# Kernel optimization log

Measured on AMD Instinct MI355X. Metric: run time of the kernel, lower is better.

The kernel has to match this reference:

```python
import jax, jax.numpy as jnp
import numpy as np

H, A, V = 8, 32, 32
NODE_IN, EDGE_IN, NODE_OUT, EDGE_OUT = 128, 64, 128, 64


def setup_inputs() -> dict:
    key = jax.random.key(0)
    ks = jax.random.split(key, 8)
    B, N = 1, 384
    s = lambda fan: 1.0 / np.sqrt(fan).astype(np.float32)
    nodes = jax.random.normal(ks[0], (B, NODE_IN, N), jnp.float32)
    edges = jax.random.normal(ks[1], (B, EDGE_IN, N, N), jnp.float32)
    mask = jax.random.randint(ks[2], (B, N), 0, 2).astype(bool)
    W_q = jax.random.normal(ks[3], (A * H, NODE_IN), jnp.float32) * s(NODE_IN)
    W_k = jax.random.normal(ks[4], (A * H, NODE_IN + EDGE_IN), jnp.float32) * s(NODE_IN + EDGE_IN)
    W_v = jax.random.normal(ks[5], (V * H, NODE_IN + EDGE_IN), jnp.float32) * s(NODE_IN + EDGE_IN)
    W_o = jax.random.normal(ks[6], (NODE_OUT, V * H), jnp.float32) * s(V * H)
    W_e = jax.random.normal(ks[7], (EDGE_OUT, V * H + EDGE_IN), jnp.float32) * s(V * H + EDGE_IN)
    return dict(nodes=nodes, edges=edges, mask=mask, W_q=W_q, W_k=W_k, W_v=W_v, W_o=W_o, W_e=W_e)


def reference(nodes, edges, mask, W_q, W_k, W_v, W_o, W_e):
    B, C, N = nodes.shape
    # 1x1 convs are channel matmuls
    query = jnp.einsum('oc,bcn->bon', W_q, nodes)                      # [B, H*A, N]
    node_edges = jnp.concatenate(
        [jnp.broadcast_to(nodes[:, :, :, None], (B, C, N, N)), edges], axis=1)  # [B, C+E, N, N]
    key = jnp.einsum('oc,bcij->boij', W_k, node_edges)                 # [B, H*A, N, N]
    value = jnp.einsum('oc,bcij->boij', W_v, node_edges).reshape(B, H, V, N, N)
    # elementwise QK: query broadcast over column axis j
    sim = (query[:, :, :, None] * key).reshape(B, H, A, N, N).sum(axis=2)
    sim = sim / jnp.sqrt(jnp.asarray(A, sim.dtype))                    # [B, H, N, N]
    sim = jnp.where(mask[:, None, None, :], sim, -jnp.inf)
    sim = jax.nn.softmax(sim, axis=-1)
    mm = (mask[:, None, :, None] & mask[:, None, None, :]).astype(sim.dtype)  # [B,1,N,N]
    sim = sim * mm
    value = value * mm[:, None]
    node_features = jnp.einsum('bhij,bhvij->bhvi', sim, value).reshape(B, H * V, N)
    node_out = jnp.einsum('od,bdn->bon', W_o, node_features)           # [B, node_out, N]
    # symmetrized edge features: (f_i + f_j) / 2, then concat raw edges
    ef = (node_features[:, :, :, None] + node_features[:, :, None, :]) * 0.5  # [B,H*V,N,N]
    ef = jnp.concatenate([ef, edges], axis=1)
    edge_out = jnp.einsum('oc,bcij->boij', W_e, ef)                    # [B, edge_out, N, N]
    return node_out, edge_out
```

## Files before the change

kernel.cpp:

```cpp
#include <hip/hip_runtime.h>
#include <math.h>

#define NN 384
#define NSQ (NN*NN)

#define WS_MASKF 0
#define WS_C1    384
#define WS_P     3456
#define WS_VN    200064
#define WS_T     298368
#define WS_GH    494976
#define WS_WT    519552
#define WS_WOT   523648
#define WS_WVE   556416
#define WS_WEN   572800

typedef short short8 __attribute__((ext_vector_type(8)));
typedef float f32x4 __attribute__((ext_vector_type(4)));

__device__ __forceinline__ unsigned short f2bf(float x) {
    unsigned u = __float_as_uint(x);
    return (unsigned short)((u + 0x7FFFu + ((u >> 16) & 1u)) >> 16);
}

__global__ __launch_bounds__(256) void k_proj(
    const float* __restrict__ nodes, const float* __restrict__ Wq,
    const float* __restrict__ Wk, const float* __restrict__ Wv,
    const float* __restrict__ Wo, const float* __restrict__ We,
    const unsigned int* __restrict__ mi, float* __restrict__ ws) {
    int tid = threadIdx.x;
    if (blockIdx.x >= 48) {
        if (blockIdx.x == 48) {
            __shared__ int bytemode;
            if (tid == 0) bytemode = 0;
            __syncthreads();
            unsigned v0 = mi[tid];
            unsigned v1 = (tid < 128) ? mi[256 + tid] : 0u;
            if (v0 > 1u || v1 > 1u) bytemode = 1;
            __syncthreads();
            float* maskf = ws + WS_MASKF;
            for (int j = tid; j < NN; j += 256) {
                int on;
                if (bytemode) on = (((const unsigned char*)mi)[j] != 0);
                else          on = (mi[j] != 0u);
                maskf[j] = on ? 1.0f : 0.0f;
            }
        } else if (blockIdx.x == 49) {
            float* Wt = ws + WS_WT;
            for (int idx = tid; idx < 4096; idx += 256) {
                int c = idx >> 6, o = idx & 63;
                Wt[c * 64 + o] = We[o * 320 + 256 + c];
            }
        } else if (blockIdx.x == 50) {
            float* WoT = ws + WS_WOT;
            for (int idx = tid; idx < 32768; idx += 256) {
                int dd = idx >> 7, o = idx & 127;
                WoT[dd * 128 + o] = Wo[o * 256 + dd];
            }
        } else if (blockIdx.x == 51) {
            float* WvE = ws + WS_WVE;
            for (int idx = tid; idx < 16384; idx += 256) {
                int c = idx >> 8, d = idx & 255;
                WvE[c * 256 + d] = Wv[d * 192 + 128 + c];
            }
        } else {
            float* WeN = ws + WS_WEN;
            for (int idx = tid; idx < 16384; idx += 256) {
                int dd = idx >> 6, o = idx & 63;
                WeN[dd * 64 + o] = We[o * 320 + dd];
            }
        }
        return;
    }
    float* c1_ws = ws + WS_C1;
    float* P_ws  = ws + WS_P;
    float* vn_ws = ws + WS_VN;
    int i0 = blockIdx.x * 8;
    __shared__ float nl[128][8];
    __shared__ float q_l[256][8];
    __shared__ float qk_l[256][8];
    for (int idx = tid; idx < 1024; idx += 256) {
        int m = idx >> 3, ii = idx & 7;
        nl[m][ii] = nodes[m * NN + i0 + ii];
    }
    __syncthreads();
    int o = tid;
    float aq[8], ak[8], av[8];
#pragma unroll
    for (int ii = 0; ii < 8; ii++) { aq[ii] = 0.f; ak[ii] = 0.f; av[ii] = 0.f; }
#pragma unroll 4
    for (int m = 0; m < 128; m++) {
        float wq = Wq[o * 128 + m];
        float wk = Wk[o * 192 + m];
        float wv = Wv[o * 192 + m];
#pragma unroll
        for (int ii = 0; ii < 8; ii++) {
            float nv = nl[m][ii];
            aq[ii] = fmaf(wq, nv, aq[ii]);
            ak[ii] = fmaf(wk, nv, ak[ii]);
            av[ii] = fmaf(wv, nv, av[ii]);
        }
    }
#pragma unroll
    for (int ii = 0; ii < 8; ii++) {
        vn_ws[(size_t)(i0 + ii) * 256 + o] = av[ii];
        q_l[o][ii]  = aq[ii];
        qk_l[o][ii] = aq[ii] * ak[ii];
    }
    __syncthreads();
    if (tid < 64) {
        int h = tid >> 3, ii = tid & 7;
        float s = 0.f;
        for (int a = 0; a < 32; a++) s += qk_l[h * 32 + a][ii];
        c1_ws[(i0 + ii) * 8 + h] = s;
    }
    for (int rep = 0; rep < 2; rep++) {
        int idx = rep * 256 + tid;
        int c = idx & 63, h = idx >> 6;
        float ap[8];
#pragma unroll
        for (int ii = 0; ii < 8; ii++) ap[ii] = 0.f;
        for (int a = 0; a < 32; a++) {
            float w = Wk[(h * 32 + a) * 192 + 128 + c];
#pragma unroll
            for (int ii = 0; ii < 8; ii++)
                ap[ii] = fmaf(q_l[h * 32 + a][ii], w, ap[ii]);
        }
#pragma unroll
        for (int ii = 0; ii < 8; ii++)
            P_ws[(size_t)(i0 + ii) * 512 + c * 8 + h] = ap[ii];
    }
}

__global__ __launch_bounds__(512) void k_attn(
    const float* __restrict__ edges, const float* __restrict__ ws_ro,
    float* __restrict__ T_ws) {
    __shared__ __align__(16) unsigned short epad_h[64 * 392];
    __shared__ __align__(16) float sT2[NN * 8];
    const float* maskf = ws_ro + WS_MASKF;
    const float* c1w   = ws_ro + WS_C1;
    const float* Pw    = ws_ro + WS_P;
    int i = blockIdx.x;
    int tid = threadIdx.x;
    int wv = tid >> 6, ln = tid & 63;
    float mask_i = maskf[i];

    if (tid < NN) {
        int j = tid;
        const float* eb = edges + (size_t)i * NN + j;
        const float* Pi = Pw + (size_t)i * 512;
        float acc[8];
#pragma unroll
        for (int h = 0; h < 8; h++) acc[h] = 0.f;
#pragma unroll
        for (int cb = 0; cb < 4; cb++) {
            float ev[16];
#pragma unroll
            for (int t = 0; t < 16; t++)
                ev[t] = eb[(size_t)(cb * 16 + t) * NSQ];
#pragma unroll
            for (int t = 0; t < 16; t++) {
                int c = cb * 16 + t;
                epad_h[c * 392 + j] = f2bf(ev[t]);
                const float* Pc = Pi + c * 8;
#pragma unroll
                for (int h = 0; h < 8; h++) acc[h] = fmaf(Pc[h], ev[t], acc[h]);
            }
        }
        float mj = maskf[j];
        const float* c1i = c1w + i * 8;
        float sv[8];
#pragma unroll
        for (int h = 0; h < 8; h++) {
            float s = (c1i[h] + acc[h]) * 0.17677669529663687f;
            sv[h] = (mj != 0.0f) ? s : -1e30f;
        }
        *reinterpret_cast<float4*>(&sT2[j * 8])     = make_float4(sv[0], sv[1], sv[2], sv[3]);
        *reinterpret_cast<float4*>(&sT2[j * 8 + 4]) = make_float4(sv[4], sv[5], sv[6], sv[7]);
    }
    __syncthreads();
    float v[6];
    {
        int h = wv;
#pragma unroll
        for (int k = 0; k < 6; k++) v[k] = sT2[(ln + 64 * k) * 8 + h];
    }
    __syncthreads();
    {
        int h = wv;
        float m = v[0];
#pragma unroll
        for (int k = 1; k < 6; k++) m = fmaxf(m, v[k]);
#pragma unroll
        for (int s = 1; s < 64; s <<= 1) m = fmaxf(m, __shfl_xor(m, s));
        float ex[6]; float sum = 0.f;
#pragma unroll
        for (int k = 0; k < 6; k++) { ex[k] = __expf(v[k] - m); sum += ex[k]; }
#pragma unroll
        for (int s = 1; s < 64; s <<= 1) sum += __shfl_xor(sum, s);
        float fac = mask_i / sum;
        unsigned short* s_bf = reinterpret_cast<unsigned short*>(sT2);
#pragma unroll
        for (int k = 0; k < 6; k++)
            s_bf[h * 392 + ln + 64 * k] = f2bf(ex[k] * fac);
    }
    __syncthreads();
    if (tid < 64) {
        const unsigned short* s_bf = reinterpret_cast<const unsigned short*>(sT2);
        int L = tid;
        int nc   = L & 15;
        int quad = L >> 4;
        int hrow = nc & 7;
        f32x4 acc0 = {0.f, 0.f, 0.f, 0.f};
        f32x4 acc1 = {0.f, 0.f, 0.f, 0.f};
        f32x4 acc2 = {0.f, 0.f, 0.f, 0.f};
        f32x4 acc3 = {0.f, 0.f, 0.f, 0.f};
#pragma unroll
        for (int s = 0; s < 12; s++) {
            int jb = s * 32 + quad * 8;
            short8 a = *reinterpret_cast<const short8*>(&s_bf[hrow * 392 + jb]);
            short8 b0 = *reinterpret_cast<const short8*>(&epad_h[(0 * 16 + nc) * 392 + jb]);
            short8 b1 = *reinterpret_cast<const short8*>(&epad_h[(1 * 16 + nc) * 392 + jb]);
            short8 b2 = *reinterpret_cast<const short8*>(&epad_h[(2 * 16 + nc) * 392 + jb]);
            short8 b3 = *reinterpret_cast<const short8*>(&epad_h[(3 * 16 + nc) * 392 + jb]);
            acc0 = __builtin_amdgcn_mfma_f32_16x16x32_bf16(a, b0, acc0, 0, 0, 0);
            acc1 = __builtin_amdgcn_mfma_f32_16x16x32_bf16(a, b1, acc1, 0, 0, 0);
            acc2 = __builtin_amdgcn_mfma_f32_16x16x32_bf16(a, b2, acc2, 0, 0, 0);
            acc3 = __builtin_amdgcn_mfma_f32_16x16x32_bf16(a, b3, acc3, 0, 0, 0);
        }
        if (L < 32) {
            float* To = T_ws + (size_t)i * 512;
#pragma unroll
            for (int r = 0; r < 4; r++) {
                int h = quad * 4 + r;
                To[h * 64 +  0 + nc] = acc0[r];
                To[h * 64 + 16 + nc] = acc1[r];
                To[h * 64 + 32 + nc] = acc2[r];
                To[h * 64 + 48 + nc] = acc3[r];
            }
        }
    }
}

__global__ __launch_bounds__(256) void k_nf(
    const float* __restrict__ ws_ro, float* __restrict__ gh_ws,
    float* __restrict__ out) {
    const float* maskf = ws_ro + WS_MASKF;
    const float* vn_ws = ws_ro + WS_VN;
    const float* T_ws  = ws_ro + WS_T;
    const float* WvE   = ws_ro + WS_WVE;
    const float* WoT   = ws_ro + WS_WOT;
    const float* WeN   = ws_ro + WS_WEN;
    int i = blockIdx.x, tid = threadIdx.x;
    __shared__ float T_l[512];
    __shared__ float nf_l[256];
    T_l[tid]       = T_ws[(size_t)i * 512 + tid];
    T_l[tid + 256] = T_ws[(size_t)i * 512 + 256 + tid];
    __syncthreads();
    int d = tid, h = d >> 5;
    float a0 = 0.f, a1 = 0.f, a2 = 0.f, a3 = 0.f;
#pragma unroll
    for (int c = 0; c < 64; c += 4) {
        a0 = fmaf(WvE[(c    ) * 256 + d], T_l[h * 64 + c    ], a0);
        a1 = fmaf(WvE[(c + 1) * 256 + d], T_l[h * 64 + c + 1], a1);
        a2 = fmaf(WvE[(c + 2) * 256 + d], T_l[h * 64 + c + 2], a2);
        a3 = fmaf(WvE[(c + 3) * 256 + d], T_l[h * 64 + c + 3], a3);
    }
    nf_l[d] = maskf[i] * vn_ws[(size_t)i * 256 + d] + ((a0 + a1) + (a2 + a3));
    __syncthreads();
    if (tid < 128) {
        int o = tid;
        float b0 = 0.f, b1 = 0.f, b2 = 0.f, b3 = 0.f;
#pragma unroll 8
        for (int dd = 0; dd < 256; dd += 4) {
            b0 = fmaf(WoT[(dd    ) * 128 + o], nf_l[dd    ], b0);
            b1 = fmaf(WoT[(dd + 1) * 128 + o], nf_l[dd + 1], b1);
            b2 = fmaf(WoT[(dd + 2) * 128 + o], nf_l[dd + 2], b2);
            b3 = fmaf(WoT[(dd + 3) * 128 + o], nf_l[dd + 3], b3);
        }
        out[o * NN + i] = (b0 + b1) + (b2 + b3);
    } else if (tid < 192) {
        int o = tid - 128;
        float b0 = 0.f, b1 = 0.f, b2 = 0.f, b3 = 0.f;
#pragma unroll 8
        for (int dd = 0; dd < 256; dd += 4) {
            b0 = fmaf(WeN[(dd    ) * 64 + o], nf_l[dd    ], b0);
            b1 = fmaf(WeN[(dd + 1) * 64 + o], nf_l[dd + 1], b1);
            b2 = fmaf(WeN[(dd + 2) * 64 + o], nf_l[dd + 2], b2);
            b3 = fmaf(WeN[(dd + 3) * 64 + o], nf_l[dd + 3], b3);
        }
        gh_ws[o * NN + i] = 0.5f * ((b0 + b1) + (b2 + b3));
    }
}

__global__ __launch_bounds__(192) void k_edge(
    const float* __restrict__ edges, const float* __restrict__ ws_ro,
    float* __restrict__ out_e) {
    const float* Wt = ws_ro + WS_WT;
    const float* gh = ws_ro + WS_GH;
    int i = blockIdx.x;
    int j = blockIdx.y * 192 + threadIdx.x;
    float eo[64];
#pragma unroll
    for (int u = 0; u < 64; u++) eo[u] = 0.f;
    const float* eb = edges + (size_t)i * NN + j;
#pragma unroll 1
    for (int cb = 0; cb < 4; cb++) {
        float ev[16];
#pragma unroll
        for (int t = 0; t < 16; t++)
            ev[t] = eb[(size_t)(cb * 16 + t) * NSQ];
#pragma unroll
        for (int t = 0; t < 16; t++) {
            const float* wr = Wt + (cb * 16 + t) * 64;
#pragma unroll
            for (int u = 0; u < 64; u++) eo[u] = fmaf(wr[u], ev[t], eo[u]);
        }
    }
    size_t ob = (size_t)i * NN + j;
    const float* gib = gh + i;
    const float* gjb = gh + j;
#pragma unroll
    for (int o = 0; o < 64; o++) {
        out_e[(size_t)o * NSQ + ob] = eo[o] + gib[(size_t)o * NN] + gjb[(size_t)o * NN];
    }
}

extern "C" void kernel_launch(void* const* d_in, const int* in_sizes, int n_in,
                              void* d_out, int out_size, void* d_ws, size_t ws_size,
                              hipStream_t stream) {
    const float* nodes = (const float*)d_in[0];
    const float* edges = (const float*)d_in[1];
    const unsigned int* mask = (const unsigned int*)d_in[2];
    const float* Wq = (const float*)d_in[3];
    const float* Wk = (const float*)d_in[4];
    const float* Wv = (const float*)d_in[5];
    const float* Wo = (const float*)d_in[6];
    const float* We = (const float*)d_in[7];
    float* out = (float*)d_out;
    float* ws  = (float*)d_ws;
    float* out_e = out + 128 * NN;

    hipLaunchKernelGGL(k_proj, dim3(53), dim3(256), 0, stream,
                       nodes, Wq, Wk, Wv, Wo, We, mask, ws);
    hipLaunchKernelGGL(k_attn, dim3(384), dim3(512), 0, stream,
                       edges, ws, ws + WS_T);
    hipLaunchKernelGGL(k_nf, dim3(384), dim3(256), 0, stream, ws,
                       ws + WS_GH, out);
    hipLaunchKernelGGL(k_edge, dim3(384, 2), dim3(192), 0, stream,
                       edges, ws, out_e);
}
```

Measured before the change: 169.2 us.

## Double-buffer edge loads in attention and edge kernels, vectorize weight loads

The attention and edge kernels now prefetch the next 16-channel block of edge values into a second register array while the current block is processed, so global-load latency overlaps with the FMAs. The projection kernel reads its weights as float4 instead of scalar loads. The edge output is written with nontemporal stores to avoid polluting cache. Costs are extra register pressure (32 values held live), which may reduce occupancy in the 64-accumulator edge kernel.

```diff
diff --git a/kernel.cpp b/kernel.cpp
--- a/kernel.cpp
+++ b/kernel.cpp
@@ -88,17 +88,29 @@
     float aq[8], ak[8], av[8];
 #pragma unroll
     for (int ii = 0; ii < 8; ii++) { aq[ii] = 0.f; ak[ii] = 0.f; av[ii] = 0.f; }
-#pragma unroll 4
-    for (int m = 0; m < 128; m++) {
-        float wq = Wq[o * 128 + m];
-        float wk = Wk[o * 192 + m];
-        float wv = Wv[o * 192 + m];
-#pragma unroll
-        for (int ii = 0; ii < 8; ii++) {
-            float nv = nl[m][ii];
-            aq[ii] = fmaf(wq, nv, aq[ii]);
-            ak[ii] = fmaf(wk, nv, ak[ii]);
-            av[ii] = fmaf(wv, nv, av[ii]);
+    {
+        const float4* wq4 = reinterpret_cast<const float4*>(Wq + o * 128);
+        const float4* wk4 = reinterpret_cast<const float4*>(Wk + o * 192);
+        const float4* wv4 = reinterpret_cast<const float4*>(Wv + o * 192);
+#pragma unroll 2
+        for (int m4 = 0; m4 < 32; m4++) {
+            float4 wq = wq4[m4];
+            float4 wk = wk4[m4];
+            float4 wv = wv4[m4];
+#pragma unroll
+            for (int s = 0; s < 4; s++) {
+                int m = m4 * 4 + s;
+                float fq = s == 0 ? wq.x : s == 1 ? wq.y : s == 2 ? wq.z : wq.w;
+                float fk = s == 0 ? wk.x : s == 1 ? wk.y : s == 2 ? wk.z : wk.w;
+                float fv = s == 0 ? wv.x : s == 1 ? wv.y : s == 2 ? wv.z : wv.w;
+#pragma unroll
+                for (int ii = 0; ii < 8; ii++) {
+                    float nv = nl[m][ii];
+                    aq[ii] = fmaf(fq, nv, aq[ii]);
+                    ak[ii] = fmaf(fk, nv, ak[ii]);
+                    av[ii] = fmaf(fv, nv, av[ii]);
+                }
+            }
         }
     }
 #pragma unroll
@@ -152,21 +164,33 @@
         float acc[8];
 #pragma unroll
         for (int h = 0; h < 8; h++) acc[h] = 0.f;
-#pragma unroll
-        for (int cb = 0; cb < 4; cb++) {
-            float ev[16];
-#pragma unroll
-            for (int t = 0; t < 16; t++)
-                ev[t] = eb[(size_t)(cb * 16 + t) * NSQ];
-#pragma unroll
-            for (int t = 0; t < 16; t++) {
-                int c = cb * 16 + t;
-                epad_h[c * 392 + j] = f2bf(ev[t]);
-                const float* Pc = Pi + c * 8;
-#pragma unroll
-                for (int h = 0; h < 8; h++) acc[h] = fmaf(Pc[h], ev[t], acc[h]);
-            }
-        }
+        float evA[16], evB[16];
+#pragma unroll
+        for (int t = 0; t < 16; t++) evA[t] = eb[(size_t)t * NSQ];
+
+#define ATTN_STEP(CUR, NXT, CB, PF)                                          \
+        {                                                                    \
+            if (PF) {                                                        \
+                _Pragma("unroll")                                            \
+                for (int t = 0; t < 16; t++)                                 \
+                    NXT[t] = eb[(size_t)(((CB) + 1) * 16 + t) * NSQ];        \
+            }                                                                \
+            _Pragma("unroll")                                                \
+            for (int t = 0; t < 16; t++) {                                   \
+                int c = (CB) * 16 + t;                                       \
+                epad_h[c * 392 + j] = f2bf(CUR[t]);                          \
+                const float* Pc = Pi + c * 8;                                \
+                _Pragma("unroll")                                            \
+                for (int h = 0; h < 8; h++)                                  \
+                    acc[h] = fmaf(Pc[h], CUR[t], acc[h]);                    \
+            }                                                                \
+        }
+        ATTN_STEP(evA, evB, 0, 1)
+        ATTN_STEP(evB, evA, 1, 1)
+        ATTN_STEP(evA, evB, 2, 1)
+        ATTN_STEP(evB, evA, 3, 0)
+#undef ATTN_STEP
+
         float mj = maskf[j];
         const float* c1i = c1w + i * 8;
         float sv[8];
@@ -304,25 +328,38 @@
 #pragma unroll
     for (int u = 0; u < 64; u++) eo[u] = 0.f;
     const float* eb = edges + (size_t)i * NN + j;
-#pragma unroll 1
-    for (int cb = 0; cb < 4; cb++) {
-        float ev[16];
-#pragma unroll
-        for (int t = 0; t < 16; t++)
-            ev[t] = eb[(size_t)(cb * 16 + t) * NSQ];
-#pragma unroll
-        for (int t = 0; t < 16; t++) {
-            const float* wr = Wt + (cb * 16 + t) * 64;
-#pragma unroll
-            for (int u = 0; u < 64; u++) eo[u] = fmaf(wr[u], ev[t], eo[u]);
-        }
-    }
+    float evA[16], evB[16];
+#pragma unroll
+    for (int t = 0; t < 16; t++) evA[t] = eb[(size_t)t * NSQ];
+
+#define EDGE_STEP(CUR, NXT, CB, PF)                                          \
+    {                                                                        \
+        if (PF) {                                                            \
+            _Pragma("unroll")                                                \
+            for (int t = 0; t < 16; t++)                                     \
+                NXT[t] = eb[(size_t)(((CB) + 1) * 16 + t) * NSQ];            \
+        }                                                                    \
+        _Pragma("unroll")                                                    \
+        for (int t = 0; t < 16; t++) {                                       \
+            const float* wr = Wt + ((CB) * 16 + t) * 64;        \
+            _Pragma("unroll")                                                \
+            for (int u = 0; u < 64; u++)                                     \
+                eo[u] = fmaf(wr[u], CUR[t], eo[u]);                          \
+        }                                                                    \
+    }
+    EDGE_STEP(evA, evB, 0, 1)
+    EDGE_STEP(evB, evA, 1, 1)
+    EDGE_STEP(evA, evB, 2, 1)
+    EDGE_STEP(evB, evA, 3, 0)
+#undef EDGE_STEP
+
     size_t ob = (size_t)i * NN + j;
     const float* gib = gh + i;
     const float* gjb = gh + j;
 #pragma unroll
     for (int o = 0; o < 64; o++) {
-        out_e[(size_t)o * NSQ + ob] = eo[o] + gib[(size_t)o * NN] + gjb[(size_t)o * NN];
+        float val = eo[o] + gib[(size_t)o * NN] + gjb[(size_t)o * NN];
+        __builtin_nontemporal_store(val, &out_e[(size_t)o * NSQ + ob]);
     }
 }
 
```

After: 189.2 us. 1.12x slower.

## Compute edge projection with bf16 MFMA via LDS-staged transposed edges

Applied to the files above, without the earlier changes.

The per-edge 64x64 channel projection moves from scalar fp32 FMAs with 64 accumulators per thread to bf16 MFMA 16x16x32 instructions. Edge values are converted to bf16 and staged transposed in shared memory, and the weight is stored pre-converted to bf16 in o-major order. Output stores become nontemporal. This removes VALU FMA work and register pressure in a memory-bound kernel, but rounds the edge inputs and weights to bf16, which lowers accuracy.

```diff
diff --git a/kernel.cpp b/kernel.cpp
--- a/kernel.cpp
+++ b/kernel.cpp
@@ -46,10 +46,10 @@
                 maskf[j] = on ? 1.0f : 0.0f;
             }
         } else if (blockIdx.x == 49) {
-            float* Wt = ws + WS_WT;
+            unsigned short* WtBF = reinterpret_cast<unsigned short*>(ws + WS_WT);
             for (int idx = tid; idx < 4096; idx += 256) {
-                int c = idx >> 6, o = idx & 63;
-                Wt[c * 64 + o] = We[o * 320 + 256 + c];
+                int o = idx >> 6, c = idx & 63;
+                WtBF[o * 64 + c] = f2bf(We[o * 320 + 256 + c]);
             }
         } else if (blockIdx.x == 50) {
             float* WoT = ws + WS_WOT;
@@ -296,33 +296,75 @@
 __global__ __launch_bounds__(192) void k_edge(
     const float* __restrict__ edges, const float* __restrict__ ws_ro,
     float* __restrict__ out_e) {
-    const float* Wt = ws_ro + WS_WT;
+    __shared__ __align__(16) unsigned short eT[192 * 72];
+    const unsigned short* WtBF = reinterpret_cast<const unsigned short*>(ws_ro + WS_WT);
     const float* gh = ws_ro + WS_GH;
-    int i = blockIdx.x;
-    int j = blockIdx.y * 192 + threadIdx.x;
-    float eo[64];
-#pragma unroll
-    for (int u = 0; u < 64; u++) eo[u] = 0.f;
-    const float* eb = edges + (size_t)i * NN + j;
-#pragma unroll 1
-    for (int cb = 0; cb < 4; cb++) {
-        float ev[16];
-#pragma unroll
-        for (int t = 0; t < 16; t++)
-            ev[t] = eb[(size_t)(cb * 16 + t) * NSQ];
-#pragma unroll
-        for (int t = 0; t < 16; t++) {
-            const float* wr = Wt + (cb * 16 + t) * 64;
-#pragma unroll
-            for (int u = 0; u < 64; u++) eo[u] = fmaf(wr[u], ev[t], eo[u]);
-        }
-    }
-    size_t ob = (size_t)i * NN + j;
-    const float* gib = gh + i;
-    const float* gjb = gh + j;
-#pragma unroll
-    for (int o = 0; o < 64; o++) {
-        out_e[(size_t)o * NSQ + ob] = eo[o] + gib[(size_t)o * NN] + gjb[(size_t)o * NN];
+    int i = blockIdx.x, jh = blockIdx.y, tid = threadIdx.x;
+
+    {
+        const float* eb = edges + (size_t)i * NN + jh * 192 + tid;
+#pragma unroll
+        for (int cb = 0; cb < 4; cb++) {
+            float ev[16];
+#pragma unroll
+            for (int t = 0; t < 16; t++)
+                ev[t] = eb[(size_t)(cb * 16 + t) * NSQ];
+            short8 p0, p1;
+#pragma unroll
+            for (int t = 0; t < 8; t++) p0[t] = (short)f2bf(ev[t]);
+#pragma unroll
+            for (int t = 0; t < 8; t++) p1[t] = (short)f2bf(ev[t + 8]);
+            *reinterpret_cast<short8*>(&eT[tid * 72 + cb * 16])     = p0;
+            *reinterpret_cast<short8*>(&eT[tid * 72 + cb * 16 + 8]) = p1;
+        }
+    }
+    __syncthreads();
+
+    int L = tid & 63, wv = tid >> 6;
+    int nc = L & 15, quad = L >> 4;
+    short8 a00 = *reinterpret_cast<const short8*>(&WtBF[(0 * 16 + nc) * 64 + 0  + quad * 8]);
+    short8 a01 = *reinterpret_cast<const short8*>(&WtBF[(0 * 16 + nc) * 64 + 32 + quad * 8]);
+    short8 a10 = *reinterpret_cast<const short8*>(&WtBF[(1 * 16 + nc) * 64 + 0  + quad * 8]);
+    short8 a11 = *reinterpret_cast<const short8*>(&WtBF[(1 * 16 + nc) * 64 + 32 + quad * 8]);
+    short8 a20 = *reinterpret_cast<const short8*>(&WtBF[(2 * 16 + nc) * 64 + 0  + quad * 8]);
+    short8 a21 = *reinterpret_cast<const short8*>(&WtBF[(2 * 16 + nc) * 64 + 32 + quad * 8]);
+    short8 a30 = *reinterpret_cast<const short8*>(&WtBF[(3 * 16 + nc) * 64 + 0  + quad * 8]);
+    short8 a31 = *reinterpret_cast<const short8*>(&WtBF[(3 * 16 + nc) * 64 + 32 + quad * 8]);
+    float ghi[16];
+#pragma unroll
+    for (int ot = 0; ot < 4; ot++)
+#pragma unroll
+        for (int r = 0; r < 4; r++)
+            ghi[ot * 4 + r] = gh[(ot * 16 + quad * 4 + r) * NN + i];
+
+#pragma unroll
+    for (int jj = 0; jj < 4; jj++) {
+        int jt = wv * 4 + jj;
+        short8 b0 = *reinterpret_cast<const short8*>(&eT[(jt * 16 + nc) * 72 + 0  + quad * 8]);
+        short8 b1 = *reinterpret_cast<const short8*>(&eT[(jt * 16 + nc) * 72 + 32 + quad * 8]);
+        int j = jh * 192 + jt * 16 + nc;
+        f32x4 c0 = {0.f, 0.f, 0.f, 0.f};
+        f32x4 c1 = {0.f, 0.f, 0.f, 0.f};
+        f32x4 c2 = {0.f, 0.f, 0.f, 0.f};
+        f32x4 c3 = {0.f, 0.f, 0.f, 0.f};
+        c0 = __builtin_amdgcn_mfma_f32_16x16x32_bf16(a00, b0, c0, 0, 0, 0);
+        c0 = __builtin_amdgcn_mfma_f32_16x16x32_bf16(a01, b1, c0, 0, 0, 0);
+        c1 = __builtin_amdgcn_mfma_f32_16x16x32_bf16(a10, b0, c1, 0, 0, 0);
+        c1 = __builtin_amdgcn_mfma_f32_16x16x32_bf16(a11, b1, c1, 0, 0, 0);
+        c2 = __builtin_amdgcn_mfma_f32_16x16x32_bf16(a20, b0, c2, 0, 0, 0);
+        c2 = __builtin_amdgcn_mfma_f32_16x16x32_bf16(a21, b1, c2, 0, 0, 0);
+        c3 = __builtin_amdgcn_mfma_f32_16x16x32_bf16(a30, b0, c3, 0, 0, 0);
+        c3 = __builtin_amdgcn_mfma_f32_16x16x32_bf16(a31, b1, c3, 0, 0, 0);
+#pragma unroll
+        for (int ot = 0; ot < 4; ot++) {
+            f32x4 cc = ot == 0 ? c0 : ot == 1 ? c1 : ot == 2 ? c2 : c3;
+#pragma unroll
+            for (int r = 0; r < 4; r++) {
+                int o = ot * 16 + quad * 4 + r;
+                float val = cc[r] + ghi[ot * 4 + r] + gh[o * NN + j];
+                __builtin_nontemporal_store(val, &out_e[(size_t)o * NSQ + (size_t)i * NN + j]);
+            }
+        }
     }
 }
 
```

New measurement: 159.4 us. -5.8%, faster.
